# Kernel tuning notes

Measured on AMD Instinct MI355X. Metric: run time of the kernel, lower is better.

Reference implementation:

```python
import jax, jax.numpy as jnp
import numpy as np
import math

N = 8192  # base points
M = 8192  # target points
FEAT = 5
DESC = 4
HID = 32


def setup_inputs() -> dict:
    key = jax.random.key(0)
    ks = jax.random.split(key, 16)
    s = lambda fan_in: 1.0 / np.sqrt(fan_in)
    return {
        "base_pos": jax.random.normal(ks[0], (N, 2), jnp.float32),
        "base_feat": jax.random.normal(ks[1], (N, FEAT), jnp.float32),
        "base_desc": jax.random.normal(ks[2], (DESC,), jnp.float32),
        "target_pos": jax.random.normal(ks[3], (M, 2), jnp.float32),
        "target_feat": jax.random.normal(ks[4], (M, FEAT), jnp.float32),
        "target_desc": jax.random.normal(ks[5], (DESC,), jnp.float32),
        # NodeWeightNet MLP params (Linear(5,32) -> ReLU -> Linear(32,1))
        "w1": jax.random.uniform(ks[6], (FEAT, HID), jnp.float32, -s(FEAT), s(FEAT)),
        "b1": jax.random.uniform(ks[7], (HID,), jnp.float32, -s(FEAT), s(FEAT)),
        "w2": jax.random.uniform(ks[8], (HID, 1), jnp.float32, -s(HID), s(HID)),
        "b2": jax.random.uniform(ks[9], (1,), jnp.float32, -s(HID), s(HID)),
        # descriptor gate params (Linear(4,32) -> ReLU -> Linear(32,1))
        "g1": jax.random.uniform(ks[10], (DESC, HID), jnp.float32, -s(DESC), s(DESC)),
        "gb1": jax.random.uniform(ks[11], (HID,), jnp.float32, -s(DESC), s(DESC)),
        "g2": jax.random.uniform(ks[12], (HID, 1), jnp.float32, -s(HID), s(HID)),
        "gb2": jax.random.uniform(ks[13], (1,), jnp.float32, -s(HID), s(HID)),
        "log_sigma": jnp.asarray(math.log(0.1), jnp.float32),
        "log_scale": jnp.zeros((2,), jnp.float32),
        "bias": jnp.zeros((1,), jnp.float32),
    }


def _node_weights(feat, w1, b1, w2, b2):
    logits = jax.nn.relu(feat @ w1 + b1) @ w2 + b2  # [N,1]
    w = jax.nn.softplus(logits) + 1e-6
    return (w / w.sum())[:, 0]  # [N], sums to 1


def _mmd_term(x, wx, y, wy, inv_two_sigma2):
    # weighted sum of Gaussian kernel over all pairs, via sq-dist expansion
    d2 = (
        (x * x).sum(-1)[:, None]
        + (y * y).sum(-1)[None, :]
        - 2.0 * (x @ y.T)
    )
    k = jnp.exp(-d2 * inv_two_sigma2)
    return jnp.einsum("i,ij,j->", wx, k, wy)


def reference(base_pos, base_feat, base_desc, target_pos, target_feat, target_desc,
              w1, b1, w2, b2, g1, gb1, g2, gb2, log_sigma, log_scale, bias):
    scale = jnp.exp(log_scale)
    bp = base_pos * scale
    tp = target_pos * scale
    sigma = jnp.exp(log_sigma)
    bw = _node_weights(base_feat, w1, b1, w2, b2)
    tw = _node_weights(target_feat, w1, b1, w2, b2)
    # center=True: subtract each cloud's weighted mean
    bp = bp - (bw[:, None] * bp).sum(0)
    tp = tp - (tw[:, None] * tp).sum(0)
    inv = 1.0 / (2.0 * sigma * sigma)
    loss = (
        _mmd_term(bp, bw, bp, bw, inv)
        - 2.0 * _mmd_term(bp, bw, tp, tw, inv)
        + _mmd_term(tp, tw, tp, tw, inv)
    )
    diff = jnp.abs(base_desc - target_desc)  # [4]
    gate = jax.nn.softplus(jax.nn.relu(diff @ g1 + gb1) @ g2 + gb2) + 1e-6  # [1]
    return loss * gate.squeeze() + bias.squeeze()
```

## Files before the change

kernel.cpp:

```cpp
#include <hip/hip_runtime.h>
#include <math.h>


#define WK_THREADS 256
#define MMD_THREADS 256
#define I_PT 4
#define IB (MMD_THREADS * I_PT)
#define JB 128

__device__ __forceinline__ float softplusf(float x) {
    return fmaxf(x, 0.0f) + log1pf(expf(-fabsf(x)));
}

__device__ __forceinline__ float fast_exp2(float x) {
#if __has_builtin(__builtin_amdgcn_exp2f)
    return __builtin_amdgcn_exp2f(x);
#else
    return exp2f(x);
#endif
}

__global__ __launch_bounds__(WK_THREADS) void weight_kernel(
    const float* __restrict__ bpos, const float* __restrict__ bfeat,
    const float* __restrict__ tpos, const float* __restrict__ tfeat,
    const float* __restrict__ w1, const float* __restrict__ b1,
    const float* __restrict__ w2, const float* __restrict__ b2,
    const float* __restrict__ log_sigma, const float* __restrict__ log_scale,
    float4* __restrict__ b4, float4* __restrict__ t4,
    float* __restrict__ wpart, int n, int m)
{
    __shared__ float s_w1[160], s_b1[32], s_w2[32];
    int tid = threadIdx.x;
    if (tid < 160) s_w1[tid] = w1[tid];
    if (tid < 32) { s_b1[tid] = b1[tid]; s_w2[tid] = w2[tid]; }
    __syncthreads();

    int idx = blockIdx.x * WK_THREADS + tid;
    int total = n + m;
    float w = 0.f, px = 0.f, py = 0.f;
    int cloud = 0;
    if (idx < total) {
        const float* pos; const float* feat; int i;
        if (idx < n) { pos = bpos; feat = bfeat; i = idx; cloud = 0; }
        else         { pos = tpos; feat = tfeat; i = idx - n; cloud = 1; }
        float sigma = expf(log_sigma[0]);
        float u = 0.8493218003f / sigma;
        float sx = expf(log_scale[0]) * u;
        float sy = expf(log_scale[1]) * u;
        px = pos[2*i]   * sx;
        py = pos[2*i+1] * sy;
        float f0 = feat[5*i], f1 = feat[5*i+1], f2 = feat[5*i+2],
              f3 = feat[5*i+3], f4 = feat[5*i+4];
        float logit = b2[0];
        #pragma unroll
        for (int h = 0; h < 32; ++h) {
            float a = s_b1[h];
            a = fmaf(f0, s_w1[h],      a);
            a = fmaf(f1, s_w1[32+h],   a);
            a = fmaf(f2, s_w1[64+h],   a);
            a = fmaf(f3, s_w1[96+h],   a);
            a = fmaf(f4, s_w1[128+h],  a);
            a = fmaxf(a, 0.f);
            logit = fmaf(a, s_w2[h], logit);
        }
        w = softplusf(logit) + 1e-6f;
        float h_i = -fmaf(px, px, py * py);
        float4 v = make_float4(px, py, h_i, w);
        if (cloud == 0) b4[i] = v; else t4[i] = v;
    }
    float sw = w, swx = w * px, swy = w * py;
    #pragma unroll
    for (int off = 32; off > 0; off >>= 1) {
        sw  += __shfl_down(sw,  off, 64);
        swx += __shfl_down(swx, off, 64);
        swy += __shfl_down(swy, off, 64);
    }
    if ((tid & 63) == 0) {
        int wgid = blockIdx.x * (WK_THREADS / 64) + (tid >> 6);
        float* dst = wpart + wgid * 6;
        bool valid = (idx < total);
        float z = valid ? 1.f : 0.f;
        if (cloud == 0) {
            dst[0] = sw * z; dst[1] = swx * z; dst[2] = swy * z;
            dst[3] = 0.f;    dst[4] = 0.f;     dst[5] = 0.f;
        } else {
            dst[0] = 0.f;    dst[1] = 0.f;     dst[2] = 0.f;
            dst[3] = sw * z; dst[4] = swx * z; dst[5] = swy * z;
        }
    }
}

__device__ __forceinline__ void reduce_wpart(const float* __restrict__ wpart,
                                             int nslots, float out[6])
{
    __shared__ float lds6[4][6];
    float v[6];
    #pragma unroll
    for (int k = 0; k < 6; ++k) v[k] = 0.f;
    for (int s = threadIdx.x; s < nslots; s += blockDim.x) {
        #pragma unroll
        for (int k = 0; k < 6; ++k) v[k] += wpart[s * 6 + k];
    }
    #pragma unroll
    for (int off = 32; off > 0; off >>= 1) {
        #pragma unroll
        for (int k = 0; k < 6; ++k) v[k] += __shfl_down(v[k], off, 64);
    }
    if ((threadIdx.x & 63) == 0) {
        #pragma unroll
        for (int k = 0; k < 6; ++k) lds6[threadIdx.x >> 6][k] = v[k];
    }
    __syncthreads();
    #pragma unroll
    for (int k = 0; k < 6; ++k)
        out[k] = lds6[0][k] + lds6[1][k] + lds6[2][k] + lds6[3][k];
    __syncthreads();
}

__global__ __launch_bounds__(MMD_THREADS) void mmd_kernel(
    const float4* __restrict__ b4, const float4* __restrict__ t4,
    const float* __restrict__ wpart, int nwslots,
    float* __restrict__ partial, int n, int m, int gx, int gy)
{
    int t = blockIdx.z;
    const float4* X; const float4* Y; int nx, ny;
    if (t == 0)      { X = b4; Y = b4; nx = n; ny = n; }
    else if (t == 1) { X = b4; Y = t4; nx = n; ny = m; }
    else             { X = t4; Y = t4; nx = m; ny = m; }

    int slot = (t * gy + blockIdx.y) * gx + blockIdx.x;
    int ibase = blockIdx.x * IB;
    int j0 = blockIdx.y * JB;
    if (ibase >= nx || j0 >= ny) {
        if (threadIdx.x == 0) partial[slot] = 0.f;
        return;
    }

    float dx0 = 0.f, dy0 = 0.f;
    if (t == 1) {
        float o[6];
        reduce_wpart(wpart, nwslots, o);
        dx0 = o[1] / o[0] - o[4] / o[3];
        dy0 = o[2] / o[0] - o[5] / o[3];
    }

    __shared__ float4 ytile[JB];
    if (threadIdx.x < JB) {
        int jj = j0 + threadIdx.x;
        ytile[threadIdx.x] = (jj < ny) ? Y[jj] : make_float4(0.f, 0.f, 0.f, 0.f);
    }
    __syncthreads();

    float x2[I_PT], y2[I_PT], hi_[I_PT], wi[I_PT], acc[I_PT];
    #pragma unroll
    for (int s = 0; s < I_PT; ++s) {
        int ii = ibase + s * MMD_THREADS + threadIdx.x;
        float4 v = (ii < nx) ? X[ii] : make_float4(0.f, 0.f, 0.f, 0.f);
        float xc = v.x - dx0, yc = v.y - dy0;
        x2[s] = xc + xc;
        y2[s] = yc + yc;
        hi_[s] = -fmaf(xc, xc, yc * yc);
        wi[s] = v.w;
        acc[s] = 0.f;
    }

    int jn = min(JB, ny - j0);
    #pragma unroll 2
    for (int j = 0; j < jn; ++j) {
        float4 q = ytile[j];
        #pragma unroll
        for (int s = 0; s < I_PT; ++s) {
            float u = hi_[s] + q.z;
            u = fmaf(x2[s], q.x, u);
            u = fmaf(y2[s], q.y, u);
            acc[s] = fmaf(q.w, fast_exp2(u), acc[s]);
        }
    }
    float r = 0.f;
    #pragma unroll
    for (int s = 0; s < I_PT; ++s) r = fmaf(wi[s], acc[s], r);

    #pragma unroll
    for (int off = 32; off > 0; off >>= 1) r += __shfl_down(r, off, 64);
    __shared__ float wsum[MMD_THREADS / 64];
    if ((threadIdx.x & 63) == 0) wsum[threadIdx.x >> 6] = r;
    __syncthreads();
    if (threadIdx.x == 0) {
        float tot = 0.f;
        #pragma unroll
        for (int k = 0; k < MMD_THREADS / 64; ++k) tot += wsum[k];
        partial[slot] = tot;
    }
}

__global__ __launch_bounds__(256) void final_kernel(
    const float* __restrict__ bdesc, const float* __restrict__ tdesc,
    const float* __restrict__ g1, const float* __restrict__ gb1,
    const float* __restrict__ g2, const float* __restrict__ gb2,
    const float* __restrict__ bias, const float* __restrict__ wpart, int nwslots,
    const float* __restrict__ partial, int gx, int gy,
    float* __restrict__ out)
{
    float o[6];
    reduce_wpart(wpart, nwslots, o);
    float sb = o[0], st = o[3];

    int np1 = gx * gy;
    float p0 = 0.f, p1 = 0.f, p2 = 0.f;
    for (int k = threadIdx.x; k < 3 * np1; k += 256) {
        float v = partial[k];
        int term = k / np1;
        if (term == 0) p0 += v; else if (term == 1) p1 += v; else p2 += v;
    }
    #pragma unroll
    for (int off = 32; off > 0; off >>= 1) {
        p0 += __shfl_down(p0, off, 64);
        p1 += __shfl_down(p1, off, 64);
        p2 += __shfl_down(p2, off, 64);
    }
    __shared__ float lds3[4][3];
    if ((threadIdx.x & 63) == 0) {
        lds3[threadIdx.x >> 6][0] = p0;
        lds3[threadIdx.x >> 6][1] = p1;
        lds3[threadIdx.x >> 6][2] = p2;
    }
    __syncthreads();
    float P0 = lds3[0][0] + lds3[1][0] + lds3[2][0] + lds3[3][0];
    float P1 = lds3[0][1] + lds3[1][1] + lds3[2][1] + lds3[3][1];
    float P2 = lds3[0][2] + lds3[1][2] + lds3[2][2] + lds3[3][2];

    float a = 0.f;
    if (threadIdx.x < 32) {
        int h = threadIdx.x;
        float d0 = fabsf(bdesc[0] - tdesc[0]);
        float d1 = fabsf(bdesc[1] - tdesc[1]);
        float d2 = fabsf(bdesc[2] - tdesc[2]);
        float d3 = fabsf(bdesc[3] - tdesc[3]);
        float v = gb1[h];
        v = fmaf(d0, g1[h],      v);
        v = fmaf(d1, g1[32+h],   v);
        v = fmaf(d2, g1[64+h],   v);
        v = fmaf(d3, g1[96+h],   v);
        a = fmaxf(v, 0.f) * g2[h];
    }
    #pragma unroll
    for (int off = 16; off > 0; off >>= 1) a += __shfl_down(a, off, 64);
    if (threadIdx.x == 0) {
        float gate = softplusf(a + gb2[0]) + 1e-6f;
        float loss = P0 / (sb * sb) - 2.f * P1 / (sb * st) + P2 / (st * st);
        out[0] = loss * gate + bias[0];
    }
}

extern "C" void kernel_launch(void* const* d_in, const int* in_sizes, int n_in,
                              void* d_out, int out_size, void* d_ws, size_t ws_size,
                              hipStream_t stream)
{
    const float* bpos      = (const float*)d_in[0];
    const float* bfeat     = (const float*)d_in[1];
    const float* bdesc     = (const float*)d_in[2];
    const float* tpos      = (const float*)d_in[3];
    const float* tfeat     = (const float*)d_in[4];
    const float* tdesc     = (const float*)d_in[5];
    const float* w1        = (const float*)d_in[6];
    const float* b1        = (const float*)d_in[7];
    const float* w2        = (const float*)d_in[8];
    const float* b2        = (const float*)d_in[9];
    const float* g1        = (const float*)d_in[10];
    const float* gb1       = (const float*)d_in[11];
    const float* g2        = (const float*)d_in[12];
    const float* gb2       = (const float*)d_in[13];
    const float* log_sigma = (const float*)d_in[14];
    const float* log_scale = (const float*)d_in[15];
    const float* bias      = (const float*)d_in[16];
    float* out = (float*)d_out;

    int n = in_sizes[0] / 2;
    int m = in_sizes[3] / 2;

    int wb = (n + m + WK_THREADS - 1) / WK_THREADS;
    int nwslots = wb * (WK_THREADS / 64);
    int nmax = n > m ? n : m;
    int gx = (nmax + IB - 1) / IB;
    int gy = (nmax + JB - 1) / JB;

    char* ws = (char*)d_ws;
    float4* b4    = (float4*)ws;
    float4* t4    = (float4*)(ws + (size_t)n * sizeof(float4));
    float* wpart  = (float*)(ws + (size_t)(n + m) * sizeof(float4));
    float* partial = wpart + (size_t)nwslots * 6;

    weight_kernel<<<wb, WK_THREADS, 0, stream>>>(
        bpos, bfeat, tpos, tfeat, w1, b1, w2, b2, log_sigma, log_scale,
        b4, t4, wpart, n, m);

    dim3 grid(gx, gy, 3);
    mmd_kernel<<<grid, MMD_THREADS, 0, stream>>>(
        b4, t4, wpart, nwslots, partial, n, m, gx, gy);

    final_kernel<<<1, 256, 0, stream>>>(
        bdesc, tdesc, g1, gb1, g2, gb2, bias, wpart, nwslots,
        partial, gx, gy, out);
}
```

Measured before the change: 126.5 us.

## Exploit kernel symmetry in self MMD terms to compute only upper triangle

For the base-base and target-target terms, blocks entirely below the diagonal are skipped and diagonal blocks mask pairs with j <= i. The final reduction doubles the off-diagonal sum and adds the sum of squared weights, which the weight kernel now accumulates. This removes roughly half of the exp work in the two self terms, at the cost of a per-pair mask on diagonal tiles and uneven block workloads.

New measurement: 126.0 us (median of 2 runs). No clear change (-0.4%).

```diff
diff --git a/kernel.cpp b/kernel.cpp
--- a/kernel.cpp
+++ b/kernel.cpp
@@ -68,52 +68,52 @@
         float4 v = make_float4(px, py, h_i, w);
         if (cloud == 0) b4[i] = v; else t4[i] = v;
     }
-    float sw = w, swx = w * px, swy = w * py;
+    float sw = w, swx = w * px, swy = w * py, sw2 = w * w;
     #pragma unroll
     for (int off = 32; off > 0; off >>= 1) {
         sw  += __shfl_down(sw,  off, 64);
         swx += __shfl_down(swx, off, 64);
         swy += __shfl_down(swy, off, 64);
+        sw2 += __shfl_down(sw2, off, 64);
     }
     if ((tid & 63) == 0) {
         int wgid = blockIdx.x * (WK_THREADS / 64) + (tid >> 6);
-        float* dst = wpart + wgid * 6;
-        bool valid = (idx < total);
-        float z = valid ? 1.f : 0.f;
+        float* dst = wpart + wgid * 8;
+        float z = (idx < total) ? 1.f : 0.f;
         if (cloud == 0) {
-            dst[0] = sw * z; dst[1] = swx * z; dst[2] = swy * z;
-            dst[3] = 0.f;    dst[4] = 0.f;     dst[5] = 0.f;
+            dst[0] = sw * z; dst[1] = swx * z; dst[2] = swy * z; dst[3] = sw2 * z;
+            dst[4] = 0.f;    dst[5] = 0.f;     dst[6] = 0.f;     dst[7] = 0.f;
         } else {
-            dst[0] = 0.f;    dst[1] = 0.f;     dst[2] = 0.f;
-            dst[3] = sw * z; dst[4] = swx * z; dst[5] = swy * z;
+            dst[0] = 0.f;    dst[1] = 0.f;     dst[2] = 0.f;     dst[3] = 0.f;
+            dst[4] = sw * z; dst[5] = swx * z; dst[6] = swy * z; dst[7] = sw2 * z;
         }
     }
 }
 
 __device__ __forceinline__ void reduce_wpart(const float* __restrict__ wpart,
-                                             int nslots, float out[6])
-{
-    __shared__ float lds6[4][6];
-    float v[6];
-    #pragma unroll
-    for (int k = 0; k < 6; ++k) v[k] = 0.f;
+                                             int nslots, float out[8])
+{
+    __shared__ float lds8[4][8];
+    float v[8];
+    #pragma unroll
+    for (int k = 0; k < 8; ++k) v[k] = 0.f;
     for (int s = threadIdx.x; s < nslots; s += blockDim.x) {
         #pragma unroll
-        for (int k = 0; k < 6; ++k) v[k] += wpart[s * 6 + k];
+        for (int k = 0; k < 8; ++k) v[k] += wpart[s * 8 + k];
     }
     #pragma unroll
     for (int off = 32; off > 0; off >>= 1) {
         #pragma unroll
-        for (int k = 0; k < 6; ++k) v[k] += __shfl_down(v[k], off, 64);
+        for (int k = 0; k < 8; ++k) v[k] += __shfl_down(v[k], off, 64);
     }
     if ((threadIdx.x & 63) == 0) {
         #pragma unroll
-        for (int k = 0; k < 6; ++k) lds6[threadIdx.x >> 6][k] = v[k];
-    }
-    __syncthreads();
-    #pragma unroll
-    for (int k = 0; k < 6; ++k)
-        out[k] = lds6[0][k] + lds6[1][k] + lds6[2][k] + lds6[3][k];
+        for (int k = 0; k < 8; ++k) lds8[threadIdx.x >> 6][k] = v[k];
+    }
+    __syncthreads();
+    #pragma unroll
+    for (int k = 0; k < 8; ++k)
+        out[k] = lds8[0][k] + lds8[1][k] + lds8[2][k] + lds8[3][k];
     __syncthreads();
 }
 
@@ -131,17 +131,18 @@
     int slot = (t * gy + blockIdx.y) * gx + blockIdx.x;
     int ibase = blockIdx.x * IB;
     int j0 = blockIdx.y * JB;
-    if (ibase >= nx || j0 >= ny) {
+    bool same = (t != 1);
+    if (ibase >= nx || j0 >= ny || (same && j0 < ibase)) {
         if (threadIdx.x == 0) partial[slot] = 0.f;
         return;
     }
 
     float dx0 = 0.f, dy0 = 0.f;
     if (t == 1) {
-        float o[6];
+        float o[8];
         reduce_wpart(wpart, nwslots, o);
-        dx0 = o[1] / o[0] - o[4] / o[3];
-        dy0 = o[2] / o[0] - o[5] / o[3];
+        dx0 = o[1] / o[0] - o[5] / o[4];
+        dy0 = o[2] / o[0] - o[6] / o[4];
     }
 
     __shared__ float4 ytile[JB];
@@ -152,9 +153,11 @@
     __syncthreads();
 
     float x2[I_PT], y2[I_PT], hi_[I_PT], wi[I_PT], acc[I_PT];
+    int ii_[I_PT];
     #pragma unroll
     for (int s = 0; s < I_PT; ++s) {
         int ii = ibase + s * MMD_THREADS + threadIdx.x;
+        ii_[s] = ii;
         float4 v = (ii < nx) ? X[ii] : make_float4(0.f, 0.f, 0.f, 0.f);
         float xc = v.x - dx0, yc = v.y - dy0;
         x2[s] = xc + xc;
@@ -165,15 +168,32 @@
     }
 
     int jn = min(JB, ny - j0);
-    #pragma unroll 2
-    for (int j = 0; j < jn; ++j) {
-        float4 q = ytile[j];
-        #pragma unroll
-        for (int s = 0; s < I_PT; ++s) {
-            float u = hi_[s] + q.z;
-            u = fmaf(x2[s], q.x, u);
-            u = fmaf(y2[s], q.y, u);
-            acc[s] = fmaf(q.w, fast_exp2(u), acc[s]);
+    if (same && j0 < ibase + IB) {
+        #pragma unroll 2
+        for (int j = 0; j < jn; ++j) {
+            float4 q = ytile[j];
+            int jj = j0 + j;
+            #pragma unroll
+            for (int s = 0; s < I_PT; ++s) {
+                float u = hi_[s] + q.z;
+                u = fmaf(x2[s], q.x, u);
+                u = fmaf(y2[s], q.y, u);
+                float e = fast_exp2(u);
+                float qw = (jj > ii_[s]) ? q.w : 0.f;
+                acc[s] = fmaf(qw, e, acc[s]);
+            }
+        }
+    } else {
+        #pragma unroll 2
+        for (int j = 0; j < jn; ++j) {
+            float4 q = ytile[j];
+            #pragma unroll
+            for (int s = 0; s < I_PT; ++s) {
+                float u = hi_[s] + q.z;
+                u = fmaf(x2[s], q.x, u);
+                u = fmaf(y2[s], q.y, u);
+                acc[s] = fmaf(q.w, fast_exp2(u), acc[s]);
+            }
         }
     }
     float r = 0.f;
@@ -201,9 +221,10 @@
     const float* __restrict__ partial, int gx, int gy,
     float* __restrict__ out)
 {
-    float o[6];
+    float o[8];
     reduce_wpart(wpart, nwslots, o);
-    float sb = o[0], st = o[3];
+    float sb = o[0], st = o[4];
+    float sw2b = o[3], sw2t = o[7];
 
     int np1 = gx * gy;
     float p0 = 0.f, p1 = 0.f, p2 = 0.f;
@@ -228,6 +249,9 @@
     float P0 = lds3[0][0] + lds3[1][0] + lds3[2][0] + lds3[3][0];
     float P1 = lds3[0][1] + lds3[1][1] + lds3[2][1] + lds3[3][1];
     float P2 = lds3[0][2] + lds3[1][2] + lds3[2][2] + lds3[3][2];
+
+    float T0 = 2.f * P0 + sw2b;
+    float T2 = 2.f * P2 + sw2t;
 
     float a = 0.f;
     if (threadIdx.x < 32) {
@@ -247,7 +271,7 @@
     for (int off = 16; off > 0; off >>= 1) a += __shfl_down(a, off, 64);
     if (threadIdx.x == 0) {
         float gate = softplusf(a + gb2[0]) + 1e-6f;
-        float loss = P0 / (sb * sb) - 2.f * P1 / (sb * st) + P2 / (st * st);
+        float loss = T0 / (sb * sb) - 2.f * P1 / (sb * st) + T2 / (st * st);
         out[0] = loss * gate + bias[0];
     }
 }
@@ -288,7 +312,7 @@
     float4* b4    = (float4*)ws;
     float4* t4    = (float4*)(ws + (size_t)n * sizeof(float4));
     float* wpart  = (float*)(ws + (size_t)(n + m) * sizeof(float4));
-    float* partial = wpart + (size_t)nwslots * 6;
+    float* partial = wpart + (size_t)nwslots * 8;
 
     weight_kernel<<<wb, WK_THREADS, 0, stream>>>(
         bpos, bfeat, tpos, tfeat, w1, b1, w2, b2, log_sigma, log_scale,
```
